# Kernel optimization log

Measured on AMD Instinct MI355X. Metric: run time of the kernel, lower is better.

Reference implementation:

```python
import jax, jax.numpy as jnp
import numpy as np

S, DIM, H = 2048, 1024, 16
D = DIM // H  # head_dim = 64


def rope_rotate_half(x):
    x1, x2 = jnp.split(x, 2, axis=-1)
    return jnp.concatenate([-x2, x1], axis=-1)


def setup_inputs() -> dict:
    key = jax.random.key(0)
    ks = jax.random.split(key, 8)
    x = jax.random.normal(ks[0], (S, DIM), dtype=jnp.float32)
    # RoPE tables for full sequence (HW == S, prefix == 0)
    pos = jnp.arange(S, dtype=jnp.float32)[:, None]
    inv_freq = 1.0 / (10000.0 ** (jnp.arange(0, D, 2, dtype=jnp.float32) / D))
    ang = pos * inv_freq[None, :]                      # [S, D/2]
    ang = jnp.concatenate([ang, ang], axis=-1)         # [S, D]
    sin, cos = jnp.sin(ang), jnp.cos(ang)
    # equinox Linear: weight [out, in], y = W @ x + b
    W_qkv = jax.random.normal(ks[1], (3 * DIM, DIM), dtype=jnp.float32) * (DIM ** -0.5)
    b_qkv = jnp.zeros((3 * DIM,), dtype=jnp.float32)
    W_proj = jax.random.normal(ks[2], (DIM, DIM), dtype=jnp.float32) * (DIM ** -0.5)
    b_proj = jnp.zeros((DIM,), dtype=jnp.float32)
    return {"x": x, "sin": sin, "cos": cos, "W_qkv": W_qkv, "b_qkv": b_qkv,
            "W_proj": W_proj, "b_proj": b_proj}


def reference(x, sin, cos, W_qkv, b_qkv, W_proj, b_proj):
    # fused QKV projection: [S, 3*DIM]
    qkv = x @ W_qkv.T + b_qkv
    # 's (n h d) -> n h s d'
    qkv = qkv.reshape(S, 3, H, D).transpose(1, 2, 0, 3)
    q, k, v = qkv[0], qkv[1], qkv[2]                   # each [H, S, D]
    # qk_norm = False -> Identity. RoPE over all S tokens (prefix = 0).
    sin_b, cos_b = sin[None, :, :], cos[None, :, :]    # [1, S, D]
    q = q * cos_b + rope_rotate_half(q) * sin_b
    k = k * cos_b + rope_rotate_half(k) * sin_b
    attn = jnp.einsum('hqd,hkd->hqk', q, k) / jnp.sqrt(jnp.float32(D))
    attn = jax.nn.softmax(attn, axis=-1)               # [H, S, S]
    out = jnp.einsum('hqk,hkd->hqd', attn, v)          # [H, S, D]
    out = out.transpose(1, 0, 2).reshape(S, DIM)       # 'h s d -> s (h d)'
    return out @ W_proj.T + b_proj
```

## Files before the change

### kernel.cpp

```cpp
#include <hip/hip_runtime.h>

#define S_LEN 2048
#define DIM 1024
#define NH 16
#define HD 64
#define KSPLIT 4

typedef __attribute__((ext_vector_type(8))) __bf16 bf16x8;
typedef __attribute__((ext_vector_type(4))) _Float16 f16x4;
typedef __attribute__((ext_vector_type(4))) float f32x4;
typedef __attribute__((ext_vector_type(8))) unsigned short us8;
typedef __attribute__((ext_vector_type(4))) unsigned short us4;

__device__ __forceinline__ unsigned short f2bf(float f) {
    union { float f; unsigned u; } v; v.f = f;
    unsigned r = v.u + 0x7FFFu + ((v.u >> 16) & 1u);
    return (unsigned short)(r >> 16);
}
__device__ __forceinline__ float bf2f(unsigned short h) {
    union { unsigned u; float f; } v; v.u = ((unsigned)h) << 16;
    return v.f;
}
__device__ __forceinline__ f32x4 mfma16(bf16x8 a, bf16x8 b, f32x4 c) {
    return __builtin_amdgcn_mfma_f32_16x16x32_bf16(a, b, c, 0, 0, 0);
}
__device__ __forceinline__ f32x4 mfma16h(f16x4 a, f16x4 b, f32x4 c) {
    return __builtin_amdgcn_mfma_f32_16x16x16f16(a, b, c, 0, 0, 0);
}
__device__ __forceinline__ void gload_lds16(void* lds, const void* g) {
    __builtin_amdgcn_global_load_lds(
        (__attribute__((address_space(1))) void*)const_cast<void*>(g),
        (__attribute__((address_space(3))) void*)lds, 16, 0, 0);
}
__device__ __forceinline__ int sw32(int row, int c) {
    const int p = row >> 1;
    return (p * 8 + ((((row & 1) << 2) | c) ^ (p & 7))) * 8;
}
__device__ __forceinline__ int sw64(int row, int c) {
    return (row * 8 + (c ^ (row & 7))) * 8;
}

__global__ __launch_bounds__(256) void convert2_kernel(
    const float* __restrict__ a, unsigned short* __restrict__ oa,
    const float* __restrict__ b, unsigned short* __restrict__ ob)
{
    const int bid = blockIdx.x;
    const float* in;
    unsigned short* out;
    int i;
    if (bid < 1024) { in = a; out = oa; i = (bid * 256 + threadIdx.x) * 8; }
    else            { in = b; out = ob; i = ((bid - 1024) * 256 + threadIdx.x) * 8; }
    const float4 p = *(const float4*)(in + i);
    const float4 q = *(const float4*)(in + i + 4);
    us8 o;
    o[0] = f2bf(p.x); o[1] = f2bf(p.y); o[2] = f2bf(p.z); o[3] = f2bf(p.w);
    o[4] = f2bf(q.x); o[5] = f2bf(q.y); o[6] = f2bf(q.z); o[7] = f2bf(q.w);
    *(us8*)(out + i) = o;
}

__global__ __launch_bounds__(256) void gemm_qkv_fused_kernel(
    const unsigned short* __restrict__ A, const unsigned short* __restrict__ B,
    const float* __restrict__ bias, const float* __restrict__ sin_t,
    const float* __restrict__ cos_t, unsigned short* __restrict__ qkv,
    _Float16* __restrict__ Vt)
{
    __shared__ __align__(16) unsigned short As[128 * 32];
    __shared__ __align__(16) unsigned short Bs[128 * 32];

    const int tid  = threadIdx.x;
    const int w    = tid >> 6;
    const int lane = tid & 63;
    const int quad = lane >> 4;
    const int l15  = lane & 15;
    const int bm = blockIdx.y * 128, bn = blockIdx.x * 128;
    const int wm = (w >> 1) * 64,    wn = (w & 1) * 64;
    const int K = DIM;

    const int pl   = lane >> 3;
    const int tt   = (lane & 7) ^ pl;
    const int srow = (pl << 1) | (tt >> 2);
    const int skc  = (tt & 3) << 3;

    f32x4 acc[4][4];
    const f32x4 zero4 = {0.f, 0.f, 0.f, 0.f};
    #pragma unroll
    for (int i = 0; i < 4; ++i)
        #pragma unroll
        for (int j = 0; j < 4; ++j) acc[i][j] = zero4;

    for (int k0 = 0; k0 < K; k0 += 32) {
        __syncthreads();
        #pragma unroll
        for (int t = 0; t < 2; ++t) {
            const int R0 = w * 32 + t * 16;
            gload_lds16(&As[R0 * 32], A + (size_t)(bm + R0 + srow) * K + k0 + skc);
            gload_lds16(&Bs[R0 * 32], B + (size_t)(bn + R0 + srow) * K + k0 + skc);
        }
        __syncthreads();

        bf16x8 a[4], b[4];
        #pragma unroll
        for (int i = 0; i < 4; ++i) {
            a[i] = *(const bf16x8*)&As[sw32(wm + 16 * i + l15, quad)];
            b[i] = *(const bf16x8*)&Bs[sw32(wn + 16 * i + l15, quad)];
        }
        #pragma unroll
        for (int i = 0; i < 4; ++i)
            #pragma unroll
            for (int j = 0; j < 4; ++j)
                acc[i][j] = mfma16(a[i], b[j], acc[i][j]);
    }

    const int sec = blockIdx.x >> 3;
    float bv[4];
    #pragma unroll
    for (int j = 0; j < 4; ++j) bv[j] = bias[bn + wn + 16 * j + l15];

    if (sec < 2) {
        const float scale = (sec == 0) ? 0.125f : 1.0f;
        const int colb = bn + wn + l15;
        #pragma unroll
        for (int i = 0; i < 4; ++i)
            #pragma unroll
            for (int r = 0; r < 4; ++r) {
                const int row = bm + wm + 16 * i + quad * 4 + r;
                const float cv0 = cos_t[row * 64 + l15];
                const float sv0 = sin_t[row * 64 + l15];
                const float cv1 = cos_t[row * 64 + 16 + l15];
                const float sv1 = sin_t[row * 64 + 16 + l15];
                const float v0 = acc[i][0][r] + bv[0];
                const float v1 = acc[i][1][r] + bv[1];
                const float v2 = acc[i][2][r] + bv[2];
                const float v3 = acc[i][3][r] + bv[3];
                unsigned short* dst = qkv + (size_t)row * (3 * DIM) + colb;
                dst[0]  = f2bf((v0 * cv0 - v2 * sv0) * scale);
                dst[16] = f2bf((v1 * cv1 - v3 * sv1) * scale);
                dst[32] = f2bf((v2 * cv0 + v0 * sv0) * scale);
                dst[48] = f2bf((v3 * cv1 + v1 * sv1) * scale);
            }
    } else {
        const int vcolb = (blockIdx.x - 16) * 128 + wn;
        #pragma unroll
        for (int j = 0; j < 4; ++j) {
            const int vcol = vcolb + 16 * j + l15;
            const int h = vcol >> 6, d = vcol & 63;
            #pragma unroll
            for (int i = 0; i < 4; ++i) {
                const int s0 = bm + wm + 16 * i + quad * 4;
                f16x4 o;
                #pragma unroll
                for (int r = 0; r < 4; ++r)
                    o[r] = (_Float16)(acc[i][j][r] + bv[j]);
                *(f16x4*)&Vt[(size_t)h * HD * S_LEN + (size_t)d * S_LEN + s0] = o;
            }
        }
    }
}

__global__ __launch_bounds__(256, 4) void attn_mfma_kernel(
    const unsigned short* __restrict__ qkv, const unsigned short* __restrict__ VtU,
    unsigned short* __restrict__ Opart, float* __restrict__ Lpart)
{
    __shared__ __align__(16) unsigned short Ks[64 * 64];
    __shared__ __align__(16) unsigned short Vts[64 * 64];

    const int h   = blockIdx.y;
    const int qb  = blockIdx.x * 128;
    const int ks  = blockIdx.z;
    const int kb0 = ks * (S_LEN / KSPLIT);
    const int tid  = threadIdx.x;
    const int w    = tid >> 6;
    const int lane = tid & 63;
    const int quad = lane >> 4;
    const int l15  = lane & 15;
    const int t7   = l15 & 7;
    const size_t hoff = (size_t)h * S_LEN * HD;

    bf16x8 aq[2][2];
    #pragma unroll
    for (int g = 0; g < 2; ++g)
        #pragma unroll
        for (int c = 0; c < 2; ++c)
            aq[g][c] = *(const bf16x8*)
                &qkv[(size_t)(qb + w * 32 + g * 16 + l15) * (3 * DIM) +
                     h * HD + 32 * c + quad * 8];

    const f32x4 zero4 = {0.f, 0.f, 0.f, 0.f};
    f32x4 o[2][4];
    #pragma unroll
    for (int g = 0; g < 2; ++g)
        #pragma unroll
        for (int dt = 0; dt < 4; ++dt) o[g][dt] = zero4;
    float lsum[2] = {0.f, 0.f};

    const int r0 = tid >> 3;
    const int c0 = tid & 7;

    us8 pk[2], pv[2];
    #pragma unroll
    for (int i = 0; i < 2; ++i) {
        const int row = r0 + 32 * i;
        pk[i] = *(const us8*)&qkv[(size_t)(kb0 + row) * (3 * DIM) +
                                  DIM + h * HD + c0 * 8];
        pv[i] = *(const us8*)&VtU[hoff + (size_t)row * S_LEN + kb0 + c0 * 8];
    }

    for (int kb = 0; kb < S_LEN / KSPLIT; kb += 64) {
        __syncthreads();
        #pragma unroll
        for (int i = 0; i < 2; ++i) {
            const int row = r0 + 32 * i;
            const int sw  = ((c0 ^ (row & 7)) << 3);
            *(us8*)&Ks[row * 64 + sw]  = pk[i];
            *(us8*)&Vts[row * 64 + sw] = pv[i];
        }
        __syncthreads();

        if (kb + 64 < S_LEN / KSPLIT) {
            #pragma unroll
            for (int i = 0; i < 2; ++i) {
                const int row = r0 + 32 * i;
                pk[i] = *(const us8*)&qkv[(size_t)(kb0 + kb + 64 + row) * (3 * DIM) +
                                          DIM + h * HD + c0 * 8];
                pv[i] = *(const us8*)&VtU[hoff + (size_t)row * S_LEN +
                                          kb0 + kb + 64 + c0 * 8];
            }
        }

        const _Float16* VtsH = (const _Float16*)Vts;
        #pragma unroll
        for (int g = 0; g < 2; ++g) {
            f32x4 s[4];
            #pragma unroll
            for (int kt = 0; kt < 4; ++kt) s[kt] = zero4;
            #pragma unroll
            for (int c = 0; c < 2; ++c)
                #pragma unroll
                for (int kt = 0; kt < 4; ++kt) {
                    const bf16x8 kf = *(const bf16x8*)
                        &Ks[(16 * kt + l15) * 64 + (((4 * c + quad) ^ t7) << 3)];
                    s[kt] = mfma16(kf, aq[g][c], s[kt]);
                }

            f16x4 pb[4];
            #pragma unroll
            for (int kt = 0; kt < 4; ++kt)
                #pragma unroll
                for (int r = 0; r < 4; ++r) {
                    const float p = __expf(s[kt][r]);
                    lsum[g] += p;
                    pb[kt][r] = (_Float16)p;
                }

            #pragma unroll
            for (int kt = 0; kt < 4; ++kt)
                #pragma unroll
                for (int dt = 0; dt < 4; ++dt) {
                    const f16x4 vf = *(const f16x4*)
                        &VtsH[(16 * dt + l15) * 64 +
                              (((2 * kt + (quad >> 1)) ^ t7) << 3) + (quad & 1) * 4];
                    o[g][dt] = mfma16h(pb[kt], vf, o[g][dt]);
                }
        }
    }

    #pragma unroll
    for (int g = 0; g < 2; ++g) {
        lsum[g] += __shfl_xor(lsum[g], 16);
        lsum[g] += __shfl_xor(lsum[g], 32);
        if (lane < 16)
            Lpart[((size_t)ks * NH + h) * S_LEN + qb + w * 32 + g * 16 + l15] = lsum[g];
    }

    #pragma unroll
    for (int g = 0; g < 2; ++g)
        #pragma unroll
        for (int dt = 0; dt < 4; ++dt)
            #pragma unroll
            for (int r = 0; r < 4; ++r) {
                const int row = qb + w * 32 + g * 16 + quad * 4 + r;
                Opart[(size_t)ks * S_LEN * DIM + (size_t)row * DIM +
                      h * HD + 16 * dt + l15] = f2bf(o[g][dt][r]);
            }
}

__global__ __launch_bounds__(256) void combine_kernel(
    const unsigned short* __restrict__ Opart, const float* __restrict__ Lpart,
    unsigned short* __restrict__ outb,
    const float* __restrict__ Wp, unsigned short* __restrict__ wp_bf)
{
    const int bid = blockIdx.x;
    if (bid < 2048) {
        const int idx = (bid * 256 + threadIdx.x) * 4;
        const int q = idx >> 10, col = idx & 1023, h = col >> 6;
        float l = 0.f;
        float v0 = 0.f, v1 = 0.f, v2 = 0.f, v3 = 0.f;
        #pragma unroll
        for (int ks = 0; ks < KSPLIT; ++ks) {
            l += Lpart[((size_t)ks * NH + h) * S_LEN + q];
            const us4 a = *(const us4*)(Opart + (size_t)ks * S_LEN * DIM + idx);
            v0 += bf2f(a[0]); v1 += bf2f(a[1]); v2 += bf2f(a[2]); v3 += bf2f(a[3]);
        }
        const float rl = 1.0f / l;
        us4 ob;
        ob[0] = f2bf(v0 * rl); ob[1] = f2bf(v1 * rl);
        ob[2] = f2bf(v2 * rl); ob[3] = f2bf(v3 * rl);
        *(us4*)(outb + idx) = ob;
    } else {
        const int i = ((bid - 2048) * 256 + threadIdx.x) * 8;
        const float4 p = *(const float4*)(Wp + i);
        const float4 q = *(const float4*)(Wp + i + 4);
        us8 o;
        o[0] = f2bf(p.x); o[1] = f2bf(p.y); o[2] = f2bf(p.z); o[3] = f2bf(p.w);
        o[4] = f2bf(q.x); o[5] = f2bf(q.y); o[6] = f2bf(q.z); o[7] = f2bf(q.w);
        *(us8*)(wp_bf + i) = o;
    }
}

__global__ __launch_bounds__(256) void gemm_proj_kernel(
    const unsigned short* __restrict__ A, const unsigned short* __restrict__ B,
    const float* __restrict__ bias, float* __restrict__ C,
    int M, int N, int K)
{
    __shared__ __align__(16) unsigned short As[64 * 64];
    __shared__ __align__(16) unsigned short Bs[64 * 64];

    const int tid  = threadIdx.x;
    const int w    = tid >> 6;
    const int lane = tid & 63;
    const int quad = lane >> 4;
    const int l15  = lane & 15;
    const int bm = blockIdx.y * 64, bn = blockIdx.x * 64;

    f32x4 acc[4];
    const f32x4 zero4 = {0.f, 0.f, 0.f, 0.f};
    #pragma unroll
    for (int j = 0; j < 4; ++j) acc[j] = zero4;

    for (int k0 = 0; k0 < K; k0 += 64) {
        __syncthreads();
        #pragma unroll
        for (int i2 = 0; i2 < 2; ++i2) {
            const int CI  = i2 * 256 + tid;
            const int row = CI >> 3;
            const int c   = (CI & 7) ^ (row & 7);
            const int base = (i2 * 256 + w * 64) * 8;
            gload_lds16(&As[base], A + (size_t)(bm + row) * K + k0 + c * 8);
            gload_lds16(&Bs[base], B + (size_t)(bn + row) * K + k0 + c * 8);
        }
        __syncthreads();

        #pragma unroll
        for (int c32 = 0; c32 < 2; ++c32) {
            const bf16x8 a = *(const bf16x8*)&As[sw64(w * 16 + l15, c32 * 4 + quad)];
            #pragma unroll
            for (int j = 0; j < 4; ++j) {
                const bf16x8 b = *(const bf16x8*)&Bs[sw64(16 * j + l15, c32 * 4 + quad)];
                acc[j] = mfma16(a, b, acc[j]);
            }
        }
    }

    #pragma unroll
    for (int j = 0; j < 4; ++j) {
        const int col = bn + 16 * j + l15;
        const float bv = bias[col];
        #pragma unroll
        for (int r = 0; r < 4; ++r) {
            const int row = bm + w * 16 + quad * 4 + r;
            C[(size_t)row * N + col] = acc[j][r] + bv;
        }
    }
}

extern "C" void kernel_launch(void* const* d_in, const int* in_sizes, int n_in,
                              void* d_out, int out_size, void* d_ws, size_t ws_size,
                              hipStream_t stream) {
    const float* x      = (const float*)d_in[0];
    const float* sin_t  = (const float*)d_in[1];
    const float* cos_t  = (const float*)d_in[2];
    const float* W_qkv  = (const float*)d_in[3];
    const float* b_qkv  = (const float*)d_in[4];
    const float* W_proj = (const float*)d_in[5];
    const float* b_proj = (const float*)d_in[6];
    float* out = (float*)d_out;

    char* ws = (char*)d_ws;
    unsigned short* qkv_bf = (unsigned short*)(ws);
    _Float16*       Vtbf   = (_Float16*)     (ws + 12582912);
    unsigned short* Opart  = (unsigned short*)(ws + 16777216);
    float*          Lpart  = (float*)        (ws + 33554432);
    unsigned short* a_bf   = (unsigned short*)(ws + 34078720);
    unsigned short* x_bf   = (unsigned short*)(ws + 38273024);
    unsigned short* wp_bf  = (unsigned short*)(ws + 38273024);
    unsigned short* wq_bf  = (unsigned short*)(ws + 42467328);

    const dim3 blk(256);

    convert2_kernel<<<dim3(2560), blk, 0, stream>>>(x, x_bf, W_qkv, wq_bf);

    gemm_qkv_fused_kernel<<<dim3(24, 16), blk, 0, stream>>>(
        x_bf, wq_bf, b_qkv, sin_t, cos_t, qkv_bf, Vtbf);

    attn_mfma_kernel<<<dim3(16, NH, KSPLIT), blk, 0, stream>>>(
        qkv_bf, (const unsigned short*)Vtbf, Opart, Lpart);

    combine_kernel<<<dim3(2560), blk, 0, stream>>>(
        Opart, Lpart, a_bf, W_proj, wp_bf);

    gemm_proj_kernel<<<dim3(16, 32), blk, 0, stream>>>(
        a_bf, wp_bf, b_proj, out, S_LEN, DIM, DIM);
}
```

Before: 150.9 us.

## Double-buffer K/V tiles in attention and fold log2e into Q scale

```diff
diff --git a/kernel.cpp b/kernel.cpp
--- a/kernel.cpp
+++ b/kernel.cpp
@@ -39,6 +39,8 @@
 __device__ __forceinline__ int sw64(int row, int c) {
     return (row * 8 + (c ^ (row & 7))) * 8;
 }
+
+#define QSCALE 0.1803368801111904f
 
 __global__ __launch_bounds__(256) void convert2_kernel(
     const float* __restrict__ a, unsigned short* __restrict__ oa,
@@ -117,7 +119,7 @@
     for (int j = 0; j < 4; ++j) bv[j] = bias[bn + wn + 16 * j + l15];
 
     if (sec < 2) {
-        const float scale = (sec == 0) ? 0.125f : 1.0f;
+        const float scale = (sec == 0) ? QSCALE : 1.0f;
         const int colb = bn + wn + l15;
         #pragma unroll
         for (int i = 0; i < 4; ++i)
@@ -161,8 +163,8 @@
     const unsigned short* __restrict__ qkv, const unsigned short* __restrict__ VtU,
     unsigned short* __restrict__ Opart, float* __restrict__ Lpart)
 {
-    __shared__ __align__(16) unsigned short Ks[64 * 64];
-    __shared__ __align__(16) unsigned short Vts[64 * 64];
+    __shared__ __align__(16) unsigned short Ks[2][64 * 64];
+    __shared__ __align__(16) unsigned short Vts[2][64 * 64];
 
     const int h   = blockIdx.y;
     const int qb  = blockIdx.x * 128;
@@ -175,6 +177,7 @@
     const int l15  = lane & 15;
     const int t7   = l15 & 7;
     const size_t hoff = (size_t)h * S_LEN * HD;
+    const int NT = (S_LEN / KSPLIT) / 64;
 
     bf16x8 aq[2][2];
     #pragma unroll
@@ -195,6 +198,8 @@
 
     const int r0 = tid >> 3;
     const int c0 = tid & 7;
+    const int sw0 = ((c0 ^ (r0 & 7)) << 3);
+    const int sw1 = ((c0 ^ ((r0 + 32) & 7)) << 3);
 
     us8 pk[2], pv[2];
     #pragma unroll
@@ -204,30 +209,24 @@
                                   DIM + h * HD + c0 * 8];
         pv[i] = *(const us8*)&VtU[hoff + (size_t)row * S_LEN + kb0 + c0 * 8];
     }
-
-    for (int kb = 0; kb < S_LEN / KSPLIT; kb += 64) {
-        __syncthreads();
-        #pragma unroll
-        for (int i = 0; i < 2; ++i) {
-            const int row = r0 + 32 * i;
-            const int sw  = ((c0 ^ (row & 7)) << 3);
-            *(us8*)&Ks[row * 64 + sw]  = pk[i];
-            *(us8*)&Vts[row * 64 + sw] = pv[i];
-        }
-        __syncthreads();
-
-        if (kb + 64 < S_LEN / KSPLIT) {
-            #pragma unroll
-            for (int i = 0; i < 2; ++i) {
-                const int row = r0 + 32 * i;
-                pk[i] = *(const us8*)&qkv[(size_t)(kb0 + kb + 64 + row) * (3 * DIM) +
-                                          DIM + h * HD + c0 * 8];
-                pv[i] = *(const us8*)&VtU[hoff + (size_t)row * S_LEN +
-                                          kb0 + kb + 64 + c0 * 8];
-            }
-        }
-
-        const _Float16* VtsH = (const _Float16*)Vts;
+    *(us8*)&Ks[0][r0 * 64 + sw0]         = pk[0];
+    *(us8*)&Vts[0][r0 * 64 + sw0]        = pv[0];
+    *(us8*)&Ks[0][(r0 + 32) * 64 + sw1]  = pk[1];
+    *(us8*)&Vts[0][(r0 + 32) * 64 + sw1] = pv[1];
+    #pragma unroll
+    for (int i = 0; i < 2; ++i) {
+        const int row = r0 + 32 * i;
+        pk[i] = *(const us8*)&qkv[(size_t)(kb0 + 64 + row) * (3 * DIM) +
+                                  DIM + h * HD + c0 * 8];
+        pv[i] = *(const us8*)&VtU[hoff + (size_t)row * S_LEN + kb0 + 64 + c0 * 8];
+    }
+    __syncthreads();
+
+    for (int t = 0; t < NT; ++t) {
+        const int cur = t & 1;
+        const _Float16* VtsH = (const _Float16*)Vts[cur];
+        const unsigned short* Kc = Ks[cur];
+
         #pragma unroll
         for (int g = 0; g < 2; ++g) {
             f32x4 s[4];
@@ -238,7 +237,7 @@
                 #pragma unroll
                 for (int kt = 0; kt < 4; ++kt) {
                     const bf16x8 kf = *(const bf16x8*)
-                        &Ks[(16 * kt + l15) * 64 + (((4 * c + quad) ^ t7) << 3)];
+                        &Kc[(16 * kt + l15) * 64 + (((4 * c + quad) ^ t7) << 3)];
                     s[kt] = mfma16(kf, aq[g][c], s[kt]);
                 }
 
@@ -247,7 +246,7 @@
             for (int kt = 0; kt < 4; ++kt)
                 #pragma unroll
                 for (int r = 0; r < 4; ++r) {
-                    const float p = __expf(s[kt][r]);
+                    const float p = exp2f(s[kt][r]);
                     lsum[g] += p;
                     pb[kt][r] = (_Float16)p;
                 }
@@ -262,6 +261,26 @@
                     o[g][dt] = mfma16h(pb[kt], vf, o[g][dt]);
                 }
         }
+
+        if (t + 1 < NT) {
+            const int nxt = (t + 1) & 1;
+            *(us8*)&Ks[nxt][r0 * 64 + sw0]         = pk[0];
+            *(us8*)&Vts[nxt][r0 * 64 + sw0]        = pv[0];
+            *(us8*)&Ks[nxt][(r0 + 32) * 64 + sw1]  = pk[1];
+            *(us8*)&Vts[nxt][(r0 + 32) * 64 + sw1] = pv[1];
+        }
+        if (t + 2 < NT) {
+            const int kb = (t + 2) * 64;
+            #pragma unroll
+            for (int i = 0; i < 2; ++i) {
+                const int row = r0 + 32 * i;
+                pk[i] = *(const us8*)&qkv[(size_t)(kb0 + kb + row) * (3 * DIM) +
+                                          DIM + h * HD + c0 * 8];
+                pv[i] = *(const us8*)&VtU[hoff + (size_t)row * S_LEN +
+                                          kb0 + kb + c0 * 8];
+            }
+        }
+        __syncthreads();
     }
 
     #pragma unroll
```

Result: slower. 162.1 us (+7.4%).

## Fuse split-K combine into projection GEMM and use exp2 softmax

Applied to the files above, without the earlier changes.

```diff
diff --git a/kernel.cpp b/kernel.cpp
--- a/kernel.cpp
+++ b/kernel.cpp
@@ -40,16 +40,20 @@
     return (row * 8 + (c ^ (row & 7))) * 8;
 }
 
-__global__ __launch_bounds__(256) void convert2_kernel(
+#define QSCALE 0.1803368801111904f
+
+__global__ __launch_bounds__(256) void convert3_kernel(
     const float* __restrict__ a, unsigned short* __restrict__ oa,
-    const float* __restrict__ b, unsigned short* __restrict__ ob)
+    const float* __restrict__ b, unsigned short* __restrict__ ob,
+    const float* __restrict__ c, unsigned short* __restrict__ oc)
 {
     const int bid = blockIdx.x;
     const float* in;
     unsigned short* out;
     int i;
-    if (bid < 1024) { in = a; out = oa; i = (bid * 256 + threadIdx.x) * 8; }
-    else            { in = b; out = ob; i = ((bid - 1024) * 256 + threadIdx.x) * 8; }
+    if (bid < 1024)      { in = a; out = oa; i = (bid * 256 + threadIdx.x) * 8; }
+    else if (bid < 2560) { in = b; out = ob; i = ((bid - 1024) * 256 + threadIdx.x) * 8; }
+    else                 { in = c; out = oc; i = ((bid - 2560) * 256 + threadIdx.x) * 8; }
     const float4 p = *(const float4*)(in + i);
     const float4 q = *(const float4*)(in + i + 4);
     us8 o;
@@ -117,7 +121,7 @@
     for (int j = 0; j < 4; ++j) bv[j] = bias[bn + wn + 16 * j + l15];
 
     if (sec < 2) {
-        const float scale = (sec == 0) ? 0.125f : 1.0f;
+        const float scale = (sec == 0) ? QSCALE : 1.0f;
         const int colb = bn + wn + l15;
         #pragma unroll
         for (int i = 0; i < 4; ++i)
@@ -247,7 +251,7 @@
             for (int kt = 0; kt < 4; ++kt)
                 #pragma unroll
                 for (int r = 0; r < 4; ++r) {
-                    const float p = __expf(s[kt][r]);
+                    const float p = exp2f(s[kt][r]);
                     lsum[g] += p;
                     pb[kt][r] = (_Float16)p;
                 }
@@ -284,43 +288,10 @@
             }
 }
 
-__global__ __launch_bounds__(256) void combine_kernel(
+__global__ __launch_bounds__(256) void gemm_proj_kernel(
     const unsigned short* __restrict__ Opart, const float* __restrict__ Lpart,
-    unsigned short* __restrict__ outb,
-    const float* __restrict__ Wp, unsigned short* __restrict__ wp_bf)
-{
-    const int bid = blockIdx.x;
-    if (bid < 2048) {
-        const int idx = (bid * 256 + threadIdx.x) * 4;
-        const int q = idx >> 10, col = idx & 1023, h = col >> 6;
-        float l = 0.f;
-        float v0 = 0.f, v1 = 0.f, v2 = 0.f, v3 = 0.f;
-        #pragma unroll
-        for (int ks = 0; ks < KSPLIT; ++ks) {
-            l += Lpart[((size_t)ks * NH + h) * S_LEN + q];
-            const us4 a = *(const us4*)(Opart + (size_t)ks * S_LEN * DIM + idx);
-            v0 += bf2f(a[0]); v1 += bf2f(a[1]); v2 += bf2f(a[2]); v3 += bf2f(a[3]);
-        }
-        const float rl = 1.0f / l;
-        us4 ob;
-        ob[0] = f2bf(v0 * rl); ob[1] = f2bf(v1 * rl);
-        ob[2] = f2bf(v2 * rl); ob[3] = f2bf(v3 * rl);
-        *(us4*)(outb + idx) = ob;
-    } else {
-        const int i = ((bid - 2048) * 256 + threadIdx.x) * 8;
-        const float4 p = *(const float4*)(Wp + i);
-        const float4 q = *(const float4*)(Wp + i + 4);
-        us8 o;
-        o[0] = f2bf(p.x); o[1] = f2bf(p.y); o[2] = f2bf(p.z); o[3] = f2bf(p.w);
-        o[4] = f2bf(q.x); o[5] = f2bf(q.y); o[6] = f2bf(q.z); o[7] = f2bf(q.w);
-        *(us8*)(wp_bf + i) = o;
-    }
-}
-
-__global__ __launch_bounds__(256) void gemm_proj_kernel(
-    const unsigned short* __restrict__ A, const unsigned short* __restrict__ B,
-    const float* __restrict__ bias, float* __restrict__ C,
-    int M, int N, int K)
+    const unsigned short* __restrict__ B, const float* __restrict__ bias,
+    float* __restrict__ C)
 {
     __shared__ __align__(16) unsigned short As[64 * 64];
     __shared__ __align__(16) unsigned short Bs[64 * 64];
@@ -331,6 +302,7 @@
     const int quad = lane >> 4;
     const int l15  = lane & 15;
     const int bm = blockIdx.y * 64, bn = blockIdx.x * 64;
+    const int K = DIM, N = DIM;
 
     f32x4 acc[4];
     const f32x4 zero4 = {0.f, 0.f, 0.f, 0.f};
@@ -338,14 +310,30 @@
     for (int j = 0; j < 4; ++j) acc[j] = zero4;
 
     for (int k0 = 0; k0 < K; k0 += 64) {
+        const int h = k0 >> 6;
         __syncthreads();
         #pragma unroll
         for (int i2 = 0; i2 < 2; ++i2) {
             const int CI  = i2 * 256 + tid;
             const int row = CI >> 3;
             const int c   = (CI & 7) ^ (row & 7);
+            const int q   = bm + row;
+            float l = 0.f;
+            float v[8] = {0.f, 0.f, 0.f, 0.f, 0.f, 0.f, 0.f, 0.f};
+            #pragma unroll
+            for (int ks = 0; ks < KSPLIT; ++ks) {
+                l += Lpart[((size_t)ks * NH + h) * S_LEN + q];
+                const us8 a = *(const us8*)&Opart[(size_t)ks * S_LEN * DIM +
+                                                  (size_t)q * DIM + k0 + c * 8];
+                #pragma unroll
+                for (int j = 0; j < 8; ++j) v[j] += bf2f(a[j]);
+            }
+            const float rl = 1.0f / l;
+            us8 o;
+            #pragma unroll
+            for (int j = 0; j < 8; ++j) o[j] = f2bf(v[j] * rl);
+            *(us8*)&As[CI * 8] = o;
             const int base = (i2 * 256 + w * 64) * 8;
-            gload_lds16(&As[base], A + (size_t)(bm + row) * K + k0 + c * 8);
             gload_lds16(&Bs[base], B + (size_t)(bn + row) * K + k0 + c * 8);
         }
         __syncthreads();
@@ -390,14 +378,14 @@
     _Float16*       Vtbf   = (_Float16*)     (ws + 12582912);
     unsigned short* Opart  = (unsigned short*)(ws + 16777216);
     float*          Lpart  = (float*)        (ws + 33554432);
-    unsigned short* a_bf   = (unsigned short*)(ws + 34078720);
-    unsigned short* x_bf   = (unsigned short*)(ws + 38273024);
-    unsigned short* wp_bf  = (unsigned short*)(ws + 38273024);
-    unsigned short* wq_bf  = (unsigned short*)(ws + 42467328);
+    unsigned short* x_bf   = (unsigned short*)(ws + 34603008);
+    unsigned short* wq_bf  = (unsigned short*)(ws + 38797312);
+    unsigned short* wp_bf  = (unsigned short*)(ws + 45088768);
 
     const dim3 blk(256);
 
-    convert2_kernel<<<dim3(2560), blk, 0, stream>>>(x, x_bf, W_qkv, wq_bf);
+    convert3_kernel<<<dim3(3072), blk, 0, stream>>>(
+        x, x_bf, W_qkv, wq_bf, W_proj, wp_bf);
 
     gemm_qkv_fused_kernel<<<dim3(24, 16), blk, 0, stream>>>(
         x_bf, wq_bf, b_qkv, sin_t, cos_t, qkv_bf, Vtbf);
@@ -405,9 +393,6 @@
     attn_mfma_kernel<<<dim3(16, NH, KSPLIT), blk, 0, stream>>>(
         qkv_bf, (const unsigned short*)Vtbf, Opart, Lpart);
 
-    combine_kernel<<<dim3(2560), blk, 0, stream>>>(
-        Opart, Lpart, a_bf, W_proj, wp_bf);
-
     gemm_proj_kernel<<<dim3(16, 32), blk, 0, stream>>>(
-        a_bf, wp_bf, b_proj, out, S_LEN, DIM, DIM);
-}
+        Opart, Lpart, wp_bf, b_proj, out);
+}
```

Measured after the change: 206.0 us. 36.5% more time.
